# Kernel optimization log

Hardware: AMD Instinct MI355X
Metric: run time of the kernel (lower is better)

## Reference

```python
import jax, jax.numpy as jnp
import numpy as np

B, C, H, W = 4, 256, 64, 64
C8 = C // 8


def setup_inputs() -> dict:
    key = jax.random.key(0)
    ks = jax.random.split(key, 8)
    x = jax.random.normal(ks[0], (B, C, H, W), dtype=jnp.float32)
    valid = jax.random.uniform(ks[1], (B, 1, H, W), dtype=jnp.float32)
    # 1x1 conv weights (kernel_size=1 -> plain channel matmul) + biases
    Wq = jax.random.normal(ks[2], (C8, C), dtype=jnp.float32) * 0.05
    bq = jnp.zeros((C8,), dtype=jnp.float32)
    Wk = jax.random.normal(ks[3], (C8, C), dtype=jnp.float32) * 0.05
    bk = jnp.zeros((C8,), dtype=jnp.float32)
    Wv = jax.random.normal(ks[4], (C, C), dtype=jnp.float32) * 0.05
    bv = jnp.zeros((C,), dtype=jnp.float32)
    gamma = jnp.asarray(0.5, dtype=jnp.float32)  # nonzero so attention path matters
    return {"x": x, "valid": valid, "Wq": Wq, "bq": bq, "Wk": Wk, "bk": bk,
            "Wv": Wv, "bv": bv, "gamma": gamma}


def reference(x, valid, Wq, bq, Wk, bk, Wv, bv, gamma):
    b, c, h, w = x.shape
    n = h * w
    xf = x.reshape(b, c, n)                                   # [B,C,N]
    # valid is already at (H,W): nearest interpolate to same size is identity
    v = valid.reshape(b, 1, n)                                # [B,1,N]
    q = jnp.einsum('oc,bcn->bno', Wq, xf) + bq                # [B,N,C//8]
    k = jnp.einsum('oc,bcn->bon', Wk, xf) + bk[None, :, None] # [B,C//8,N]
    energy = jnp.einsum('bno,bom->bnm', q, k)                 # [B,N,N]
    attn = jax.nn.softmax(energy, axis=-1)
    va = attn * v                                             # mask columns
    scale = 1.0 / jnp.sum(va, axis=2, keepdims=True)          # per-row renorm
    sa = va * scale                                           # [B,N,N]
    pv = jnp.einsum('oc,bcn->bon', Wv, xf) + bv[None, :, None]  # [B,C,N]
    out = jnp.einsum('bon,bmn->bom', pv, sa)                  # bmm(V, A^T)
    out = out.reshape(b, c, h, w)
    return gamma * out + x, sa
```

## Files before the change

kernel.cpp:

```cpp
#include <hip/hip_runtime.h>

typedef unsigned short u16;
typedef unsigned int u32;
typedef __attribute__((ext_vector_type(8))) short short8;
typedef __attribute__((ext_vector_type(4))) float f32x4;
typedef __attribute__((ext_vector_type(2))) unsigned int u32x2;

#define BB 4
#define CC 256
#define NT 4096
#define L2E 1.4426950408889634f

__device__ __forceinline__ float b2f(u16 v) {
    union { u32 u; float f; } c; c.u = ((u32)v) << 16; return c.f;
}
__device__ __forceinline__ u16 f2b(float f) {
    union { float f; u32 u; } c; c.f = f;
    u32 u = c.u;
    return (u16)((u + 0x7fffu + ((u >> 16) & 1u)) >> 16);
}

__global__ __launch_bounds__(256) void kproj(
    const float* __restrict__ x,
    const float* __restrict__ Wq, const float* __restrict__ bq,
    const float* __restrict__ Wk, const float* __restrict__ bk,
    const float* __restrict__ Wv, const float* __restrict__ bv,
    u16* __restrict__ qh, u16* __restrict__ ql,
    u16* __restrict__ kh, u16* __restrict__ kl,
    u16* __restrict__ pvw)
{
    __shared__ __align__(16) float lA[32][68];
    __shared__ __align__(16) float lX[32][68];
    const int mt = blockIdx.x, nt = blockIdx.y, b = blockIdx.z;
    const int t = threadIdx.x;
    const int tx = t & 15, ty = t >> 4;
    const int n0 = nt * 64;

    float acc[4][4];
    #pragma unroll
    for (int i = 0; i < 4; ++i)
        #pragma unroll
        for (int j = 0; j < 4; ++j) acc[i][j] = 0.f;

    const int rA = t >> 2, kqA = (t & 3) * 8;
    const int rgA = mt * 64 + rA;
    const float* wrow;
    if (rgA < 32)      wrow = Wq + rgA * 256;
    else if (rgA < 64) wrow = Wk + (rgA - 32) * 256;
    else               wrow = Wv + (rgA - 64) * 256;
    const int kX = t >> 3, nn8 = (t & 7) * 8;
    const float* xrow = x + ((size_t)(b * CC + kX)) * NT + n0 + nn8;

    for (int k0 = 0; k0 < 256; k0 += 32) {
        f32x4 wa = *(const f32x4*)(wrow + k0 + kqA);
        f32x4 wb = *(const f32x4*)(wrow + k0 + kqA + 4);
        f32x4 xa = *(const f32x4*)(xrow + (size_t)k0 * NT);
        f32x4 xb = *(const f32x4*)(xrow + (size_t)k0 * NT + 4);
        __syncthreads();
        #pragma unroll
        for (int j = 0; j < 4; ++j) {
            lA[kqA + j    ][rA] = wa[j];
            lA[kqA + j + 4][rA] = wb[j];
        }
        *(f32x4*)&lX[kX][nn8]     = xa;
        *(f32x4*)&lX[kX][nn8 + 4] = xb;
        __syncthreads();
        #pragma unroll
        for (int k = 0; k < 32; ++k) {
            f32x4 av  = *(const f32x4*)&lA[k][ty * 4];
            f32x4 xvv = *(const f32x4*)&lX[k][tx * 4];
            #pragma unroll
            for (int i = 0; i < 4; ++i)
                #pragma unroll
                for (int j = 0; j < 4; ++j)
                    acc[i][j] = fmaf(av[i], xvv[j], acc[i][j]);
        }
    }

    #pragma unroll
    for (int i = 0; i < 4; ++i) {
        const int rg = mt * 64 + ty * 4 + i;
        float bias;
        if (rg < 32)      bias = bq[rg];
        else if (rg < 64) bias = bk[rg - 32];
        else              bias = bv[rg - 64];
        #pragma unroll
        for (int j = 0; j < 4; ++j) {
            const int n = n0 + tx * 4 + j;
            const float val = acc[i][j] + bias;
            const u16 h = f2b(val);
            const u16 l = f2b(val - b2f(h));
            if (rg < 32) {
                const size_t idx = ((size_t)(b * NT + n)) * 32 + rg;
                qh[idx] = h; ql[idx] = l;
            } else if (rg < 64) {
                const size_t idx = ((size_t)(b * NT + n)) * 32 + (rg - 32);
                kh[idx] = h; kl[idx] = l;
            } else {
                pvw[((size_t)b * CC + (rg - 64)) * NT + n] = f2b(val);
            }
        }
    }
}

__global__ __launch_bounds__(256) void kattn(
    const u16* __restrict__ qh, const u16* __restrict__ ql,
    const u16* __restrict__ kh, const u16* __restrict__ kl,
    const float* __restrict__ valid, float* __restrict__ sa)
{
    const int b    = blockIdx.y;
    const int lane = threadIdx.x & 63;
    const int wv   = threadIdx.x >> 6;
    const int r0   = (blockIdx.x * 4 + wv) * 16;
    const int quad = lane >> 4, l16 = lane & 15;

    const size_t abase = ((size_t)(b * NT + r0 + l16)) * 32 + quad * 8;
    const short8 aqh = *(const short8*)(qh + abase);
    const short8 aql = *(const short8*)(ql + abase);
    const size_t kb = (size_t)b * NT * 32 + (size_t)l16 * 32 + quad * 8;
    const float* vb = valid + b * NT + l16;
    const f32x4 zero = {0.f, 0.f, 0.f, 0.f};

    float sacc[4] = {0.f, 0.f, 0.f, 0.f};
    for (int ct = 0; ct < 256; ++ct) {
        short8 bh = *(const short8*)(kh + kb + (size_t)ct * 512);
        short8 bl = *(const short8*)(kl + kb + (size_t)ct * 512);
        float vcol = vb[ct * 16];
        f32x4 d = __builtin_amdgcn_mfma_f32_16x16x32_bf16(aqh, bh, zero, 0, 0, 0);
        d = __builtin_amdgcn_mfma_f32_16x16x32_bf16(aql, bh, d, 0, 0, 0);
        d = __builtin_amdgcn_mfma_f32_16x16x32_bf16(aqh, bl, d, 0, 0, 0);
        #pragma unroll
        for (int i = 0; i < 4; ++i)
            sacc[i] += vcol * exp2f(fminf(d[i], 60.f) * L2E);
    }
    #pragma unroll
    for (int i = 0; i < 4; ++i) {
        #pragma unroll
        for (int off = 1; off < 16; off <<= 1)
            sacc[i] += __shfl_xor(sacc[i], off, 64);
        sacc[i] = 1.0f / sacc[i];
    }
    for (int ct = 0; ct < 256; ++ct) {
        short8 bh = *(const short8*)(kh + kb + (size_t)ct * 512);
        short8 bl = *(const short8*)(kl + kb + (size_t)ct * 512);
        float vcol = vb[ct * 16];
        f32x4 d = __builtin_amdgcn_mfma_f32_16x16x32_bf16(aqh, bh, zero, 0, 0, 0);
        d = __builtin_amdgcn_mfma_f32_16x16x32_bf16(aql, bh, d, 0, 0, 0);
        d = __builtin_amdgcn_mfma_f32_16x16x32_bf16(aqh, bl, d, 0, 0, 0);
        #pragma unroll
        for (int i = 0; i < 4; ++i) {
            float val = vcol * exp2f(fminf(d[i], 60.f) * L2E) * sacc[i];
            sa[((size_t)(b * NT + r0 + quad * 4 + i)) * NT + ct * 16 + l16] = val;
        }
    }
}

__global__ __launch_bounds__(512) void kout(
    const u16* __restrict__ pvw, const float* __restrict__ sa,
    const float* __restrict__ x, const float* __restrict__ gamma,
    float* __restrict__ outp)
{
    __shared__ __align__(16) u16 lB[32][72];
    const int b    = blockIdx.y;
    const int m0   = blockIdx.x * 32;
    const int t    = threadIdx.x;
    const int lane = t & 63;
    const int wv   = t >> 6;
    const int c0   = wv * 32;
    const int quad = lane >> 4, l16 = lane & 15;

    const u16* a0p = pvw + ((size_t)(b * CC + c0 + l16)) * NT + quad * 8;
    const u16* a1p = a0p + (size_t)16 * NT;
    const int sm = t >> 4, sk = (t & 15) * 4;
    const float* sap = sa + ((size_t)(b * NT + m0 + sm)) * NT + sk;

    f32x4 acc00 = {0,0,0,0}, acc01 = {0,0,0,0}, acc10 = {0,0,0,0}, acc11 = {0,0,0,0};

    for (int k0 = 0; k0 < NT; k0 += 64) {
        f32x4 sv = *(const f32x4*)(sap + k0);
        __syncthreads();
        u32x2 packed;
        packed[0] = (u32)f2b(sv[0]) | ((u32)f2b(sv[1]) << 16);
        packed[1] = (u32)f2b(sv[2]) | ((u32)f2b(sv[3]) << 16);
        *(u32x2*)&lB[sm][sk] = packed;
        __syncthreads();
        #pragma unroll
        for (int half = 0; half < 64; half += 32) {
            short8 a0 = *(const short8*)(a0p + k0 + half);
            short8 a1 = *(const short8*)(a1p + k0 + half);
            short8 b0 = *(const short8*)&lB[l16     ][half + quad * 8];
            short8 b1 = *(const short8*)&lB[16 + l16][half + quad * 8];
            acc00 = __builtin_amdgcn_mfma_f32_16x16x32_bf16(a0, b0, acc00, 0, 0, 0);
            acc01 = __builtin_amdgcn_mfma_f32_16x16x32_bf16(a0, b1, acc01, 0, 0, 0);
            acc10 = __builtin_amdgcn_mfma_f32_16x16x32_bf16(a1, b0, acc10, 0, 0, 0);
            acc11 = __builtin_amdgcn_mfma_f32_16x16x32_bf16(a1, b1, acc11, 0, 0, 0);
        }
    }

    const float g = gamma[0];
    #pragma unroll
    for (int ai = 0; ai < 2; ++ai) {
        #pragma unroll
        for (int bi = 0; bi < 2; ++bi) {
            f32x4 acc = (ai == 0) ? ((bi == 0) ? acc00 : acc01)
                                  : ((bi == 0) ? acc10 : acc11);
            #pragma unroll
            for (int i = 0; i < 4; ++i) {
                const int c = c0 + ai * 16 + quad * 4 + i;
                const int m = m0 + bi * 16 + l16;
                const size_t idx = ((size_t)(b * CC + c)) * NT + m;
                outp[idx] = g * acc[i] + x[idx];
            }
        }
    }
}

extern "C" void kernel_launch(void* const* d_in, const int* in_sizes, int n_in,
                              void* d_out, int out_size, void* d_ws, size_t ws_size,
                              hipStream_t stream)
{
    const float* x     = (const float*)d_in[0];
    const float* valid = (const float*)d_in[1];
    const float* Wq    = (const float*)d_in[2];
    const float* bq    = (const float*)d_in[3];
    const float* Wk    = (const float*)d_in[4];
    const float* bk    = (const float*)d_in[5];
    const float* Wv    = (const float*)d_in[6];
    const float* bv    = (const float*)d_in[7];
    const float* gamma = (const float*)d_in[8];

    float* outp = (float*)d_out;
    float* sa   = outp + (size_t)BB * CC * NT;

    u16* qh  = (u16*)d_ws;
    u16* ql  = qh + (size_t)BB * NT * 32;
    u16* kh  = ql + (size_t)BB * NT * 32;
    u16* kl  = kh + (size_t)BB * NT * 32;
    u16* pvw = kl + (size_t)BB * NT * 32;

    kproj<<<dim3(5, 64, BB), 256, 0, stream>>>(x, Wq, bq, Wk, bk, Wv, bv,
                                               qh, ql, kh, kl, pvw);
    kattn<<<dim3(64, BB), 256, 0, stream>>>(qh, ql, kh, kl, valid, sa);
    kout<<<dim3(128, BB), 512, 0, stream>>>(pvw, sa, x, gamma, outp);
}
```

Before: 626.2 us.

## Split attention rows across waves and double-buffer the output GEMM's LDS tile

kattn now assigns one 16-row tile per block and splits the 4096 columns across four waves, combining the partial row sums through shared memory. This gives four times as many blocks for better occupancy and latency hiding. kout uses a larger 128-wide K tile with double-buffered, XOR-swizzled LDS and register prefetch of sa two tiles ahead, with a single barrier per step. This is meant to overlap global loads with MFMA work and cut barrier and bank-conflict overhead, at the cost of more registers and LDS.

```diff
diff --git a/kernel.cpp b/kernel.cpp
--- a/kernel.cpp
+++ b/kernel.cpp
@@ -5,6 +5,7 @@
 typedef __attribute__((ext_vector_type(8))) short short8;
 typedef __attribute__((ext_vector_type(4))) float f32x4;
 typedef __attribute__((ext_vector_type(2))) unsigned int u32x2;
+typedef __attribute__((ext_vector_type(4))) unsigned int u32x4;
 
 #define BB 4
 #define CC 256
@@ -108,11 +109,13 @@
     const u16* __restrict__ kh, const u16* __restrict__ kl,
     const float* __restrict__ valid, float* __restrict__ sa)
 {
+    __shared__ float sred[4][4][4];
     const int b    = blockIdx.y;
     const int lane = threadIdx.x & 63;
     const int wv   = threadIdx.x >> 6;
-    const int r0   = (blockIdx.x * 4 + wv) * 16;
+    const int r0   = blockIdx.x * 16;
     const int quad = lane >> 4, l16 = lane & 15;
+    const int ct0  = wv * 64;
 
     const size_t abase = ((size_t)(b * NT + r0 + l16)) * 32 + quad * 8;
     const short8 aqh = *(const short8*)(qh + abase);
@@ -122,7 +125,7 @@
     const f32x4 zero = {0.f, 0.f, 0.f, 0.f};
 
     float sacc[4] = {0.f, 0.f, 0.f, 0.f};
-    for (int ct = 0; ct < 256; ++ct) {
+    for (int ct = ct0; ct < ct0 + 64; ++ct) {
         short8 bh = *(const short8*)(kh + kb + (size_t)ct * 512);
         short8 bl = *(const short8*)(kl + kb + (size_t)ct * 512);
         float vcol = vb[ct * 16];
@@ -138,9 +141,19 @@
         #pragma unroll
         for (int off = 1; off < 16; off <<= 1)
             sacc[i] += __shfl_xor(sacc[i], off, 64);
-        sacc[i] = 1.0f / sacc[i];
-    }
-    for (int ct = 0; ct < 256; ++ct) {
+    }
+    if (l16 == 0) {
+        #pragma unroll
+        for (int i = 0; i < 4; ++i) sred[wv][quad][i] = sacc[i];
+    }
+    __syncthreads();
+    float inv[4];
+    #pragma unroll
+    for (int i = 0; i < 4; ++i)
+        inv[i] = 1.0f / (sred[0][quad][i] + sred[1][quad][i] +
+                         sred[2][quad][i] + sred[3][quad][i]);
+
+    for (int ct = ct0; ct < ct0 + 64; ++ct) {
         short8 bh = *(const short8*)(kh + kb + (size_t)ct * 512);
         short8 bl = *(const short8*)(kl + kb + (size_t)ct * 512);
         float vcol = vb[ct * 16];
@@ -149,18 +162,51 @@
         d = __builtin_amdgcn_mfma_f32_16x16x32_bf16(aqh, bl, d, 0, 0, 0);
         #pragma unroll
         for (int i = 0; i < 4; ++i) {
-            float val = vcol * exp2f(fminf(d[i], 60.f) * L2E) * sacc[i];
+            float val = vcol * exp2f(fminf(d[i], 60.f) * L2E) * inv[i];
             sa[((size_t)(b * NT + r0 + quad * 4 + i)) * NT + ct * 16 + l16] = val;
         }
     }
 }
+
+#define KOUT_BODY(CUR, T, NXA, NXB, FTA, FTB)                                  \
+  {                                                                            \
+    if ((T) + 2 < 32) {                                                        \
+      FTA = *(const f32x4*)(sap + (size_t)((T) + 2) * 128);                    \
+      FTB = *(const f32x4*)(sap + (size_t)((T) + 2) * 128 + 4);                \
+    }                                                                          \
+    if ((T) + 1 < 32) {                                                        \
+      u32 w0 = (u32)f2b(NXA[0]) | ((u32)f2b(NXA[1]) << 16);                    \
+      u32 w1 = (u32)f2b(NXA[2]) | ((u32)f2b(NXA[3]) << 16);                    \
+      u32 w2 = (u32)f2b(NXB[0]) | ((u32)f2b(NXB[1]) << 16);                    \
+      u32 w3 = (u32)f2b(NXB[2]) | ((u32)f2b(NXB[3]) << 16);                    \
+      u32x4 pk = {w0, w1, w2, w3};                                             \
+      *(u32x4*)(lbw + ((((T) + 1) & 1) * 8192)) = pk;                          \
+    }                                                                          \
+    const char* lb = lbr + (CUR) * 8192;                                       \
+    _Pragma("unroll")                                                          \
+    for (int kk = 0; kk < 128; kk += 32) {                                     \
+      short8 a0 = *(const short8*)(a0p + (size_t)(T) * 128 + kk);              \
+      short8 a1 = *(const short8*)(a1p + (size_t)(T) * 128 + kk);              \
+      const int kby = (((kk + quad * 8) * 2) ^ swz);                           \
+      short8 b0 = *(const short8*)(lb + l16 * 256 + kby);                      \
+      short8 b1 = *(const short8*)(lb + (16 + l16) * 256 + kby);               \
+      acc00 = __builtin_amdgcn_mfma_f32_16x16x32_bf16(a0, b0, acc00, 0, 0, 0); \
+      acc01 = __builtin_amdgcn_mfma_f32_16x16x32_bf16(a0, b1, acc01, 0, 0, 0); \
+      acc10 = __builtin_amdgcn_mfma_f32_16x16x32_bf16(a1, b0, acc10, 0, 0, 0); \
+      acc11 = __builtin_amdgcn_mfma_f32_16x16x32_bf16(a1, b1, acc11, 0, 0, 0); \
+    }                                                                          \
+    asm volatile("s_waitcnt lgkmcnt(0)" ::: "memory");                         \
+    __builtin_amdgcn_sched_barrier(0);                                         \
+    __builtin_amdgcn_s_barrier();                                              \
+    __builtin_amdgcn_sched_barrier(0);                                         \
+  }
 
 __global__ __launch_bounds__(512) void kout(
     const u16* __restrict__ pvw, const float* __restrict__ sa,
     const float* __restrict__ x, const float* __restrict__ gamma,
     float* __restrict__ outp)
 {
-    __shared__ __align__(16) u16 lB[32][72];
+    __shared__ __align__(16) u16 lB[2][32][128];
     const int b    = blockIdx.y;
     const int m0   = blockIdx.x * 32;
     const int t    = threadIdx.x;
@@ -168,33 +214,38 @@
     const int wv   = t >> 6;
     const int c0   = wv * 32;
     const int quad = lane >> 4, l16 = lane & 15;
+    const int swz  = (l16 & 7) << 4;
 
     const u16* a0p = pvw + ((size_t)(b * CC + c0 + l16)) * NT + quad * 8;
     const u16* a1p = a0p + (size_t)16 * NT;
-    const int sm = t >> 4, sk = (t & 15) * 4;
+    const int sm = t >> 4, sk = (t & 15) * 8;
     const float* sap = sa + ((size_t)(b * NT + m0 + sm)) * NT + sk;
+    char* lbw = ((char*)&lB[0][0][0]) + sm * 256 + ((sk * 2) ^ ((sm & 7) << 4));
+    const char* lbr = (const char*)&lB[0][0][0];
 
     f32x4 acc00 = {0,0,0,0}, acc01 = {0,0,0,0}, acc10 = {0,0,0,0}, acc11 = {0,0,0,0};
 
-    for (int k0 = 0; k0 < NT; k0 += 64) {
-        f32x4 sv = *(const f32x4*)(sap + k0);
-        __syncthreads();
-        u32x2 packed;
-        packed[0] = (u32)f2b(sv[0]) | ((u32)f2b(sv[1]) << 16);
-        packed[1] = (u32)f2b(sv[2]) | ((u32)f2b(sv[3]) << 16);
-        *(u32x2*)&lB[sm][sk] = packed;
-        __syncthreads();
-        #pragma unroll
-        for (int half = 0; half < 64; half += 32) {
-            short8 a0 = *(const short8*)(a0p + k0 + half);
-            short8 a1 = *(const short8*)(a1p + k0 + half);
-            short8 b0 = *(const short8*)&lB[l16     ][half + quad * 8];
-            short8 b1 = *(const short8*)&lB[16 + l16][half + quad * 8];
-            acc00 = __builtin_amdgcn_mfma_f32_16x16x32_bf16(a0, b0, acc00, 0, 0, 0);
-            acc01 = __builtin_amdgcn_mfma_f32_16x16x32_bf16(a0, b1, acc01, 0, 0, 0);
-            acc10 = __builtin_amdgcn_mfma_f32_16x16x32_bf16(a1, b0, acc10, 0, 0, 0);
-            acc11 = __builtin_amdgcn_mfma_f32_16x16x32_bf16(a1, b1, acc11, 0, 0, 0);
-        }
+    f32x4 pA = *(const f32x4*)(sap);
+    f32x4 pB = *(const f32x4*)(sap + 4);
+    f32x4 nA = *(const f32x4*)(sap + 128);
+    f32x4 nB = *(const f32x4*)(sap + 132);
+    {
+        u32 w0 = (u32)f2b(pA[0]) | ((u32)f2b(pA[1]) << 16);
+        u32 w1 = (u32)f2b(pA[2]) | ((u32)f2b(pA[3]) << 16);
+        u32 w2 = (u32)f2b(pB[0]) | ((u32)f2b(pB[1]) << 16);
+        u32 w3 = (u32)f2b(pB[2]) | ((u32)f2b(pB[3]) << 16);
+        u32x4 pk = {w0, w1, w2, w3};
+        *(u32x4*)(lbw) = pk;
+    }
+    asm volatile("s_waitcnt lgkmcnt(0)" ::: "memory");
+    __builtin_amdgcn_sched_barrier(0);
+    __builtin_amdgcn_s_barrier();
+    __builtin_amdgcn_sched_barrier(0);
+
+    f32x4 fA, fB;
+    for (int tt = 0; tt < 32; tt += 2) {
+        KOUT_BODY(0, tt,     nA, nB, fA, fB)
+        KOUT_BODY(1, tt + 1, fA, fB, nA, nB)
     }
 
     const float g = gamma[0];
@@ -240,6 +291,6 @@
 
     kproj<<<dim3(5, 64, BB), 256, 0, stream>>>(x, Wq, bq, Wk, bk, Wv, bv,
                                                qh, ql, kh, kl, pvw);
-    kattn<<<dim3(64, BB), 256, 0, stream>>>(qh, ql, kh, kl, valid, sa);
+    kattn<<<dim3(256, BB), 256, 0, stream>>>(qh, ql, kh, kl, valid, sa);
     kout<<<dim3(128, BB), 512, 0, stream>>>(pvw, sa, x, gamma, outp);
 }
```

Measured after the change: 534.5 us. 1.17x faster.

## Fuse attention-map computation with output bmm in one kernel

Applied to the files above, without the earlier changes.

Merges the attention kernel and the output matmul kernel. Each 512-thread block computes 32 rows of the normalized masked softmax: a first pass gets the row sums, split across waves and reduced through shared memory. A second pass recomputes the scores, writes sa to global memory, packs it to bf16 into a double-buffered, XOR-swizzled LDS tile, and feeds it straight into the PV MFMA accumulation. This drops the full re-read of the 4096x4096 fp32 sa matrix from global memory. In exchange it adds a block barrier per step and register-prefetches the K and valid data for the next step.

```diff
diff --git a/kernel.cpp b/kernel.cpp
--- a/kernel.cpp
+++ b/kernel.cpp
@@ -5,6 +5,7 @@
 typedef __attribute__((ext_vector_type(8))) short short8;
 typedef __attribute__((ext_vector_type(4))) float f32x4;
 typedef __attribute__((ext_vector_type(2))) unsigned int u32x2;
+typedef __attribute__((ext_vector_type(4))) unsigned int u32x4;
 
 #define BB 4
 #define CC 256
@@ -103,98 +104,120 @@
     }
 }
 
-__global__ __launch_bounds__(256) void kattn(
+#define FSTEP(S, CBH, CBL, CV4, NBH, NBL, NV4)                                 \
+  {                                                                            \
+    const int s_ = (S);                                                        \
+    short8 pa00 = *(const short8*)(pva + (size_t)s_ * 64);                     \
+    short8 pa01 = *(const short8*)(pva + (size_t)s_ * 64 + 32);                \
+    short8 pa10 = *(const short8*)(pva + (size_t)16 * NT + (size_t)s_ * 64);   \
+    short8 pa11 = *(const short8*)(pva + (size_t)16 * NT + (size_t)s_ * 64 + 32);\
+    if (s_ + 1 < 64) {                                                         \
+      const int ct_ = (s_ + 1) * 4 + cq;                                       \
+      NBH = *(const short8*)(kh + kbase + (size_t)ct_ * 512);                  \
+      NBL = *(const short8*)(kl + kbase + (size_t)ct_ * 512);                  \
+      NV4 = *(const f32x4*)(vbase + ct_ * 16 + quad * 4);                      \
+    }                                                                          \
+    f32x4 d = __builtin_amdgcn_mfma_f32_16x16x32_bf16(CBH, aqh, zero, 0, 0, 0);\
+    d = __builtin_amdgcn_mfma_f32_16x16x32_bf16(CBH, aql, d, 0, 0, 0);         \
+    d = __builtin_amdgcn_mfma_f32_16x16x32_bf16(CBL, aqh, d, 0, 0, 0);         \
+    f32x4 val;                                                                 \
+    _Pragma("unroll")                                                          \
+    for (int i = 0; i < 4; ++i)                                                \
+      val[i] = CV4[i] * exp2f(fminf(d[i], 60.f) * L2E) * inv;                  \
+    *(f32x4*)(sap + (size_t)s_ * 64 + cq * 16 + quad * 4) = val;               \
+    u32x2 pk;                                                                  \
+    pk[0] = (u32)f2b(val[0]) | ((u32)f2b(val[1]) << 16);                       \
+    pk[1] = (u32)f2b(val[2]) | ((u32)f2b(val[3]) << 16);                       \
+    *(u32x2*)(lwp + (s_ & 1) * 4096) = pk;                                     \
+    asm volatile("s_waitcnt lgkmcnt(0)" ::: "memory");                         \
+    __builtin_amdgcn_sched_barrier(0);                                         \
+    __builtin_amdgcn_s_barrier();                                              \
+    __builtin_amdgcn_sched_barrier(0);                                         \
+    const char* lb_ = lrp + (s_ & 1) * 4096;                                   \
+    _Pragma("unroll")                                                          \
+    for (int half = 0; half < 2; ++half) {                                     \
+      const int kby_ = ((half * 64 + quad * 16) ^ swz);                        \
+      short8 b0 = *(const short8*)(lb_ + l16 * 128 + kby_);                    \
+      short8 b1 = *(const short8*)(lb_ + (16 + l16) * 128 + kby_);             \
+      short8 a0 = half ? pa01 : pa00;                                          \
+      short8 a1 = half ? pa11 : pa10;                                          \
+      acc00 = __builtin_amdgcn_mfma_f32_16x16x32_bf16(a0, b0, acc00, 0, 0, 0); \
+      acc01 = __builtin_amdgcn_mfma_f32_16x16x32_bf16(a0, b1, acc01, 0, 0, 0); \
+      acc10 = __builtin_amdgcn_mfma_f32_16x16x32_bf16(a1, b0, acc10, 0, 0, 0); \
+      acc11 = __builtin_amdgcn_mfma_f32_16x16x32_bf16(a1, b1, acc11, 0, 0, 0); \
+    }                                                                          \
+  }
+
+__global__ __launch_bounds__(512, 4) void ksaout(
     const u16* __restrict__ qh, const u16* __restrict__ ql,
     const u16* __restrict__ kh, const u16* __restrict__ kl,
-    const float* __restrict__ valid, float* __restrict__ sa)
+    const float* __restrict__ valid, const u16* __restrict__ pvw,
+    const float* __restrict__ x, const float* __restrict__ gamma,
+    float* __restrict__ sa, float* __restrict__ outp)
 {
-    const int b    = blockIdx.y;
-    const int lane = threadIdx.x & 63;
-    const int wv   = threadIdx.x >> 6;
-    const int r0   = (blockIdx.x * 4 + wv) * 16;
-    const int quad = lane >> 4, l16 = lane & 15;
-
-    const size_t abase = ((size_t)(b * NT + r0 + l16)) * 32 + quad * 8;
-    const short8 aqh = *(const short8*)(qh + abase);
-    const short8 aql = *(const short8*)(ql + abase);
-    const size_t kb = (size_t)b * NT * 32 + (size_t)l16 * 32 + quad * 8;
-    const float* vb = valid + b * NT + l16;
-    const f32x4 zero = {0.f, 0.f, 0.f, 0.f};
-
-    float sacc[4] = {0.f, 0.f, 0.f, 0.f};
-    for (int ct = 0; ct < 256; ++ct) {
-        short8 bh = *(const short8*)(kh + kb + (size_t)ct * 512);
-        short8 bl = *(const short8*)(kl + kb + (size_t)ct * 512);
-        float vcol = vb[ct * 16];
-        f32x4 d = __builtin_amdgcn_mfma_f32_16x16x32_bf16(aqh, bh, zero, 0, 0, 0);
-        d = __builtin_amdgcn_mfma_f32_16x16x32_bf16(aql, bh, d, 0, 0, 0);
-        d = __builtin_amdgcn_mfma_f32_16x16x32_bf16(aqh, bl, d, 0, 0, 0);
-        #pragma unroll
-        for (int i = 0; i < 4; ++i)
-            sacc[i] += vcol * exp2f(fminf(d[i], 60.f) * L2E);
-    }
-    #pragma unroll
-    for (int i = 0; i < 4; ++i) {
-        #pragma unroll
-        for (int off = 1; off < 16; off <<= 1)
-            sacc[i] += __shfl_xor(sacc[i], off, 64);
-        sacc[i] = 1.0f / sacc[i];
-    }
-    for (int ct = 0; ct < 256; ++ct) {
-        short8 bh = *(const short8*)(kh + kb + (size_t)ct * 512);
-        short8 bl = *(const short8*)(kl + kb + (size_t)ct * 512);
-        float vcol = vb[ct * 16];
-        f32x4 d = __builtin_amdgcn_mfma_f32_16x16x32_bf16(aqh, bh, zero, 0, 0, 0);
-        d = __builtin_amdgcn_mfma_f32_16x16x32_bf16(aql, bh, d, 0, 0, 0);
-        d = __builtin_amdgcn_mfma_f32_16x16x32_bf16(aqh, bl, d, 0, 0, 0);
-        #pragma unroll
-        for (int i = 0; i < 4; ++i) {
-            float val = vcol * exp2f(fminf(d[i], 60.f) * L2E) * sacc[i];
-            sa[((size_t)(b * NT + r0 + quad * 4 + i)) * NT + ct * 16 + l16] = val;
-        }
-    }
-}
-
-__global__ __launch_bounds__(512) void kout(
-    const u16* __restrict__ pvw, const float* __restrict__ sa,
-    const float* __restrict__ x, const float* __restrict__ gamma,
-    float* __restrict__ outp)
-{
-    __shared__ __align__(16) u16 lB[32][72];
+    __shared__ __align__(16) u16 lB[2][32][64];
+    __shared__ float sred[2][4][16];
     const int b    = blockIdx.y;
     const int m0   = blockIdx.x * 32;
     const int t    = threadIdx.x;
     const int lane = t & 63;
     const int wv   = t >> 6;
-    const int c0   = wv * 32;
     const int quad = lane >> 4, l16 = lane & 15;
-
-    const u16* a0p = pvw + ((size_t)(b * CC + c0 + l16)) * NT + quad * 8;
-    const u16* a1p = a0p + (size_t)16 * NT;
-    const int sm = t >> 4, sk = (t & 15) * 4;
-    const float* sap = sa + ((size_t)(b * NT + m0 + sm)) * NT + sk;
+    const int rg   = wv >> 2, cq = wv & 3;
+    const int swz  = (l16 & 7) << 4;
+
+    const size_t qbase = ((size_t)(b * NT + m0 + rg * 16 + l16)) * 32 + quad * 8;
+    const short8 aqh = *(const short8*)(qh + qbase);
+    const short8 aql = *(const short8*)(ql + qbase);
+    const size_t kbase = (size_t)b * NT * 32 + (size_t)l16 * 32 + quad * 8;
+    const float* vbase = valid + (size_t)b * NT;
+    const f32x4 zero = {0.f, 0.f, 0.f, 0.f};
+
+    float sacc = 0.f;
+    {
+        short8 nbh = *(const short8*)(kh + kbase + (size_t)(cq * 64) * 512);
+        short8 nbl = *(const short8*)(kl + kbase + (size_t)(cq * 64) * 512);
+        f32x4  nv4 = *(const f32x4*)(vbase + (cq * 64) * 16 + quad * 4);
+        for (int s = 0; s < 64; ++s) {
+            short8 bh = nbh, bl = nbl;
+            f32x4 v4 = nv4;
+            if (s + 1 < 64) {
+                const int ct = cq * 64 + s + 1;
+                nbh = *(const short8*)(kh + kbase + (size_t)ct * 512);
+                nbl = *(const short8*)(kl + kbase + (size_t)ct * 512);
+                nv4 = *(const f32x4*)(vbase + ct * 16 + quad * 4);
+            }
+            f32x4 d = __builtin_amdgcn_mfma_f32_16x16x32_bf16(bh, aqh, zero, 0, 0, 0);
+            d = __builtin_amdgcn_mfma_f32_16x16x32_bf16(bh, aql, d, 0, 0, 0);
+            d = __builtin_amdgcn_mfma_f32_16x16x32_bf16(bl, aqh, d, 0, 0, 0);
+            #pragma unroll
+            for (int i = 0; i < 4; ++i)
+                sacc += v4[i] * exp2f(fminf(d[i], 60.f) * L2E);
+        }
+    }
+    sacc += __shfl_xor(sacc, 16, 64);
+    sacc += __shfl_xor(sacc, 32, 64);
+    if (lane < 16) sred[rg][cq][l16] = sacc;
+    __syncthreads();
+    const float inv = 1.0f / (sred[rg][0][l16] + sred[rg][1][l16] +
+                              sred[rg][2][l16] + sred[rg][3][l16]);
+
+    const u16* pva = pvw + ((size_t)(b * CC + wv * 32 + l16)) * NT + quad * 8;
+    float* sap = sa + ((size_t)(b * NT + m0 + rg * 16 + l16)) * NT;
+    char* lwp = (char*)&lB[0][0][0] + (rg * 16 + l16) * 128
+              + ((cq * 32 + quad * 8) ^ swz);
+    const char* lrp = (const char*)&lB[0][0][0];
 
     f32x4 acc00 = {0,0,0,0}, acc01 = {0,0,0,0}, acc10 = {0,0,0,0}, acc11 = {0,0,0,0};
 
-    for (int k0 = 0; k0 < NT; k0 += 64) {
-        f32x4 sv = *(const f32x4*)(sap + k0);
-        __syncthreads();
-        u32x2 packed;
-        packed[0] = (u32)f2b(sv[0]) | ((u32)f2b(sv[1]) << 16);
-        packed[1] = (u32)f2b(sv[2]) | ((u32)f2b(sv[3]) << 16);
-        *(u32x2*)&lB[sm][sk] = packed;
-        __syncthreads();
-        #pragma unroll
-        for (int half = 0; half < 64; half += 32) {
-            short8 a0 = *(const short8*)(a0p + k0 + half);
-            short8 a1 = *(const short8*)(a1p + k0 + half);
-            short8 b0 = *(const short8*)&lB[l16     ][half + quad * 8];
-            short8 b1 = *(const short8*)&lB[16 + l16][half + quad * 8];
-            acc00 = __builtin_amdgcn_mfma_f32_16x16x32_bf16(a0, b0, acc00, 0, 0, 0);
-            acc01 = __builtin_amdgcn_mfma_f32_16x16x32_bf16(a0, b1, acc01, 0, 0, 0);
-            acc10 = __builtin_amdgcn_mfma_f32_16x16x32_bf16(a1, b0, acc10, 0, 0, 0);
-            acc11 = __builtin_amdgcn_mfma_f32_16x16x32_bf16(a1, b1, acc11, 0, 0, 0);
-        }
+    short8 cbh = *(const short8*)(kh + kbase + (size_t)cq * 512);
+    short8 cbl = *(const short8*)(kl + kbase + (size_t)cq * 512);
+    f32x4  cv4 = *(const f32x4*)(vbase + cq * 16 + quad * 4);
+    short8 nbh, nbl; f32x4 nv4;
+
+    for (int s = 0; s < 64; s += 2) {
+        FSTEP(s,     cbh, cbl, cv4, nbh, nbl, nv4)
+        FSTEP(s + 1, nbh, nbl, nv4, cbh, cbl, cv4)
     }
 
     const float g = gamma[0];
@@ -206,7 +229,7 @@
                                   : ((bi == 0) ? acc10 : acc11);
             #pragma unroll
             for (int i = 0; i < 4; ++i) {
-                const int c = c0 + ai * 16 + quad * 4 + i;
+                const int c = wv * 32 + ai * 16 + quad * 4 + i;
                 const int m = m0 + bi * 16 + l16;
                 const size_t idx = ((size_t)(b * CC + c)) * NT + m;
                 outp[idx] = g * acc[i] + x[idx];
@@ -240,6 +263,6 @@
 
     kproj<<<dim3(5, 64, BB), 256, 0, stream>>>(x, Wq, bq, Wk, bk, Wv, bv,
                                                qh, ql, kh, kl, pvw);
-    kattn<<<dim3(64, BB), 256, 0, stream>>>(qh, ql, kh, kl, valid, sa);
-    kout<<<dim3(128, BB), 512, 0, stream>>>(pvw, sa, x, gamma, outp);
-}
+    ksaout<<<dim3(128, BB), 512, 0, stream>>>(qh, ql, kh, kl, valid, pvw,
+                                              x, gamma, sa, outp);
+}
```

Result: faster. 531.4 us (-15.1%).
